# Kernel tuning notes

Hardware: AMD Instinct MI355X
Metric: run time of the kernel (lower is better)

## Reference

```python
import jax, jax.numpy as jnp
import numpy as np

B, T, E = 4, 2048, 1024
H = 16
D = E // H  # head_dim = 64


def setup_inputs() -> dict:
    key = jax.random.key(0)
    k1, k2, k3 = jax.random.split(key, 3)
    x = jax.random.normal(k1, (B, T, E), dtype=jnp.float32)
    # torch nn.Linear weights: y = x @ W.T ; init scaled like uniform fan_in
    W_qkv = jax.random.normal(k2, (3 * E, E), dtype=jnp.float32) * (E ** -0.5)
    W_out = jax.random.normal(k3, (E, E), dtype=jnp.float32) * (E ** -0.5)
    return {"x": x, "W_qkv": W_qkv, "W_out": W_out}


def reference(x, W_qkv, W_out):
    b, t, c = x.shape
    scale = D ** -0.5
    qkv = jnp.einsum('btc,fc->btf', x, W_qkv)          # [B,T,3E]
    q, k, v = jnp.split(qkv, 3, axis=-1)
    # [B,H,T,D]
    q = q.reshape(b, t, H, D).transpose(0, 2, 1, 3)
    k = k.reshape(b, t, H, D).transpose(0, 2, 1, 3)
    v = v.reshape(b, t, H, D).transpose(0, 2, 1, 3)
    attn = jnp.einsum('bhqd,bhkd->bhqk', q, k) * scale  # [B,H,T,T]
    causal = jnp.triu(jnp.ones((t, t), dtype=bool), k=1)
    attn = jnp.where(causal, -jnp.inf, attn)
    attn = jax.nn.softmax(attn, axis=-1)
    out = jnp.einsum('bhqk,bhkd->bhqd', attn, v)        # [B,H,T,D]
    out = out.transpose(0, 2, 1, 3).reshape(b, t, c)
    return jnp.einsum('btc,oc->bto', out, W_out)
```

## Files before the change

### kernel.cpp

```cpp
#include <hip/hip_runtime.h>

using u16 = unsigned short;
using u32 = unsigned int;
typedef __bf16 bf16;
typedef bf16 bf16x8 __attribute__((ext_vector_type(8)));
typedef u16 u16x8 __attribute__((ext_vector_type(8)));
typedef u16 u16x4 __attribute__((ext_vector_type(4)));
typedef u32 u32x2 __attribute__((ext_vector_type(2)));
typedef float f32x4 __attribute__((ext_vector_type(4)));

#define LDSS 72

__device__ __forceinline__ u16 f2bf(float f) {
  u32 u = __builtin_bit_cast(u32, f);
  u += 0x7FFFu + ((u >> 16) & 1u);
  return (u16)(u >> 16);
}

__device__ __forceinline__ u32 packtrunc(float lo, float hi) {
  return __builtin_amdgcn_perm(__builtin_bit_cast(u32, hi),
                               __builtin_bit_cast(u32, lo), 0x07060302u);
}

__device__ __forceinline__ float fexp2(float x) {
#if __has_builtin(__builtin_amdgcn_exp2f)
  return __builtin_amdgcn_exp2f(x);
#else
  return exp2f(x);
#endif
}

__device__ __forceinline__ bf16x8 ldfrag(const u16* p) {
  return __builtin_bit_cast(bf16x8, *(const u16x8*)p);
}

__device__ __forceinline__ u16x8 cvt8(const float* p) {
  float4 a = ((const float4*)p)[0];
  float4 b = ((const float4*)p)[1];
  u16x8 o;
  o[0] = f2bf(a.x); o[1] = f2bf(a.y); o[2] = f2bf(a.z); o[3] = f2bf(a.w);
  o[4] = f2bf(b.x); o[5] = f2bf(b.y); o[6] = f2bf(b.z); o[7] = f2bf(b.w);
  return o;
}

__device__ __forceinline__ void gll16(const u16* g, u16* l) {
  __builtin_amdgcn_global_load_lds(
      (const __attribute__((address_space(1))) u32*)g,
      (__attribute__((address_space(3))) u32*)l, 16, 0, 0);
}

__global__ __launch_bounds__(256) void cvt_bf16(
    const float* __restrict__ src, u16* __restrict__ dst, int n8) {
  int i = blockIdx.x * 256 + threadIdx.x;
  const int stride = gridDim.x * 256;
  for (; i < n8; i += stride)
    ((u16x8*)dst)[i] = cvt8(&src[(size_t)i * 8]);
}

template<int MODE, int NBX>
__global__ __launch_bounds__(512, 2) void gemm256(
    const u16* __restrict__ Ag, const u16* __restrict__ Bg,
    u16* __restrict__ Qw, u16* __restrict__ Kw, u16* __restrict__ Vtw,
    float* __restrict__ Og) {
  extern __shared__ u16 lds[];
  u16* Ab0 = lds;
  u16* Bb0 = lds + 16384;
  u16* Ab1 = lds + 32768;
  u16* Bb1 = lds + 49152;

  const int tid = threadIdx.x;
  const int lane = tid & 63;
  const int wid = tid >> 6;
  const int wm = wid >> 2, wn = wid & 3;
  const int quad = lane >> 4, l16 = lane & 15;
  const int row_off = lane >> 3;
  const int csrc = ((lane & 7) * 8) ^ (row_off << 3);
  const int swl = (l16 & 7) << 3;

  const int cpx = (NBX * 32) >> 3;
  const int bid = blockIdx.x;
  const int swz = (bid & 7) * cpx + (bid >> 3);
  const int by = swz / NBX, bx = swz % NBX;
  const int arow0 = by * 256, brow0 = bx * 256;

  f32x4 acc[8][4] = {};
  bf16x8 af[8];
  bf16x8 bfx[4];

  auto stg = [&](const u16* G, int grow0, u16* dst, int t, int h) {
#pragma unroll
    for (int q = 0; q < 2; ++q) {
      int r = h * 128 + q * 64 + wid * 8;
      gll16(&G[(size_t)(grow0 + r + row_off) * 1024 + t * 64 + csrc],
            &dst[r * 64]);
    }
  };

#define LOADA(BUF, MH) do { \
  _Pragma("unroll") for (int i2 = 0; i2 < 4; ++i2) \
  _Pragma("unroll") for (int kk = 0; kk < 2; ++kk) \
    af[i2*2+kk] = ldfrag(&BUF[(wm*128 + ((MH)*4+i2)*16 + l16)*64 + ((kk*32+quad*8) ^ swl)]); \
} while(0)

#define LOADB(BUF, NH) do { \
  _Pragma("unroll") for (int j2 = 0; j2 < 2; ++j2) \
  _Pragma("unroll") for (int kk = 0; kk < 2; ++kk) \
    bfx[j2*2+kk] = ldfrag(&BUF[(wn*64 + ((NH)*2+j2)*16 + l16)*64 + ((kk*32+quad*8) ^ swl)]); \
} while(0)

#define MFMAQ(MH, NH) do { \
  __builtin_amdgcn_s_setprio(1); \
  _Pragma("unroll") for (int i2 = 0; i2 < 4; ++i2) \
  _Pragma("unroll") for (int j2 = 0; j2 < 2; ++j2) \
  _Pragma("unroll") for (int kk = 0; kk < 2; ++kk) \
    acc[(MH)*4+i2][(NH)*2+j2] = __builtin_amdgcn_mfma_f32_16x16x32_bf16( \
        af[i2*2+kk], bfx[j2*2+kk], acc[(MH)*4+i2][(NH)*2+j2], 0, 0, 0); \
  __builtin_amdgcn_s_setprio(0); \
} while(0)

#define BARSYNC __builtin_amdgcn_s_barrier()
#define LGKM0 do { asm volatile("s_waitcnt lgkmcnt(0)" ::: "memory"); \
                   __builtin_amdgcn_sched_barrier(0); } while(0)

  stg(Ag, arow0, Ab0, 0, 0);
  stg(Bg, brow0, Bb0, 0, 1);
  stg(Ag, arow0, Ab0, 0, 1);
  stg(Bg, brow0, Bb0, 0, 0);
  stg(Ag, arow0, Ab1, 1, 0);
  stg(Bg, brow0, Bb1, 1, 1);
  asm volatile("s_waitcnt vmcnt(4)" ::: "memory");
  BARSYNC;

  for (int i = 0; i < 8; ++i) {
    const int t1 = 2 * i + 1, t2 = 2 * i + 2, t3 = 2 * i + 3;
    const bool more = (i < 7);
    LOADA(Ab0, 0); LOADB(Bb0, 0); stg(Ag, arow0, Ab1, t1, 1);
    BARSYNC; LGKM0; MFMAQ(0, 0); BARSYNC;
    LOADB(Bb0, 1); stg(Bg, brow0, Bb1, t1, 0);
    BARSYNC; LGKM0; MFMAQ(0, 1); BARSYNC;
    LOADA(Ab0, 1); if (more) stg(Ag, arow0, Ab0, t2, 0);
    BARSYNC; LGKM0; MFMAQ(1, 1); BARSYNC;
    LOADB(Bb0, 0);
    if (more) { stg(Bg, brow0, Bb0, t2, 1);
                asm volatile("s_waitcnt vmcnt(4)" ::: "memory"); }
    else      { asm volatile("s_waitcnt vmcnt(0)" ::: "memory"); }
    BARSYNC; LGKM0; MFMAQ(1, 0); BARSYNC;
    LOADA(Ab1, 0); LOADB(Bb1, 0); if (more) stg(Ag, arow0, Ab0, t2, 1);
    BARSYNC; LGKM0; MFMAQ(0, 0); BARSYNC;
    LOADB(Bb1, 1); if (more) stg(Bg, brow0, Bb0, t2, 0);
    BARSYNC; LGKM0; MFMAQ(0, 1); BARSYNC;
    LOADA(Ab1, 1); if (more) stg(Ag, arow0, Ab1, t3, 0);
    BARSYNC; LGKM0; MFMAQ(1, 1); BARSYNC;
    LOADB(Bb1, 0);
    if (more) { stg(Bg, brow0, Bb1, t3, 1);
                asm volatile("s_waitcnt vmcnt(4)" ::: "memory"); }
    BARSYNC; LGKM0; MFMAQ(1, 0); BARSYNC;
  }

  if constexpr (MODE == 0) {
    const int part = bx >> 2;
    const int h = (bx & 3) * 4 + wn;
    const int bb = by >> 3;
    const int tb0 = (by & 7) * 256 + wm * 128;
    if (part < 2) {
      u16* dst = part == 0 ? Qw : Kw;
      const float qs = part == 0 ? 0.18033688011112042f : 1.0f;
      const size_t rowb = (size_t)(bb * 16 + h) * 2048;
#pragma unroll
      for (int i2 = 0; i2 < 8; ++i2)
#pragma unroll
        for (int j2 = 0; j2 < 4; ++j2) {
          int t = tb0 + i2 * 16 + quad * 4;
          int d = j2 * 16 + l16;
#pragma unroll
          for (int r = 0; r < 4; ++r)
            dst[(rowb + t + r) * 64 + d] = f2bf(acc[i2][j2][r] * qs);
        }
    } else {
      __builtin_amdgcn_s_barrier();
      u16* tb = lds + wid * 8192;
      const int swt = l16 << 2;
#pragma unroll
      for (int i2 = 0; i2 < 8; ++i2)
#pragma unroll
        for (int j2 = 0; j2 < 4; ++j2) {
          u16x4 v4;
#pragma unroll
          for (int r = 0; r < 4; ++r) v4[r] = f2bf(acc[i2][j2][r]);
          int mb = i2 * 16 + quad * 4;
          *(u16x4*)&tb[(j2 * 16 + l16) * 128 + (mb ^ swt)] = v4;
        }
      asm volatile("s_waitcnt lgkmcnt(0)" ::: "memory");
      const int dl = lane;
      const int swr = (dl & 15) << 2;
      u16* vr = Vtw + ((size_t)(bb * 16 + h) * 64 + dl) * 2048 + tb0;
#pragma unroll
      for (int c = 0; c < 16; ++c) {
        u16x4 q0 = *(u16x4*)&tb[dl * 128 + ((c * 8) ^ swr)];
        u16x4 q1 = *(u16x4*)&tb[dl * 128 + ((c * 8 + 4) ^ swr)];
        u16x8 o;
        o[0] = q0[0]; o[1] = q0[1]; o[2] = q0[2]; o[3] = q0[3];
        o[4] = q1[0]; o[5] = q1[1]; o[6] = q1[2]; o[7] = q1[3];
        *(u16x8*)&vr[c * 8] = o;
      }
    }
  } else {
    const size_t mrow = (size_t)(by * 256 + wm * 128);
    const int ocol = bx * 256 + wn * 64;
#pragma unroll
    for (int i2 = 0; i2 < 8; ++i2)
#pragma unroll
      for (int j2 = 0; j2 < 4; ++j2)
#pragma unroll
        for (int r = 0; r < 4; ++r)
          Og[(mrow + i2 * 16 + quad * 4 + r) * 1024 + ocol + j2 * 16 + l16] =
              acc[i2][j2][r];
  }
#undef LOADA
#undef LOADB
#undef MFMAQ
#undef BARSYNC
#undef LGKM0
}

__global__ __launch_bounds__(256) void attn_kernel(
    const u16* __restrict__ Qw, const u16* __restrict__ Kw,
    const u16* __restrict__ Vtw, u16* __restrict__ Ao) {
  __shared__ u16 kbuf0[64 * 64], vbuf0[64 * 64];
  __shared__ u16 kbuf1[64 * 64], vbuf1[64 * 64];
  __shared__ u16 pws[4][32 * LDSS];
  const int tid = threadIdx.x;
  const int lane = tid & 63;
  const int wid = tid >> 6;
  const int quad = lane >> 4;
  const int l16 = lane & 15;
  const int g = 15 - (int)(blockIdx.x >> 6);
  const int bh = blockIdx.x & 63;
  const u16* Qb = Qw + (size_t)bh * 2048 * 64;
  const u16* Kb = Kw + (size_t)bh * 2048 * 64;
  const u16* Vb = Vtw + (size_t)bh * 64 * 2048;
  const int sw = 4 * g + wid;
  const int qrow0 = sw * 32;
  const int nktw = (sw >> 1) + 1;
  const int nkt = 2 * g + 2;
  u16* pw = pws[wid];

  const int lr = lane >> 3;
  const int lsw = ((lane & 7) * 8) ^ (lr << 3);
  const int sx = (l16 & 7) << 3;

  bf16x8 qf[2][2];
#pragma unroll
  for (int i = 0; i < 2; ++i)
#pragma unroll
    for (int kk = 0; kk < 2; ++kk)
      qf[i][kk] = ldfrag(&Qb[(size_t)(qrow0 + i * 16 + l16) * 64 + kk * 32 + quad * 8]);

  f32x4 oacc[4][2] = {};
  float mst[2] = {-INFINITY, -INFINITY};
  float lst[2] = {0.f, 0.f};

  auto stage = [&](int kt, u16* kb, u16* vb) {
    const u16* Kt = Kb + (size_t)kt * 4096;
    const u16* Vt = Vb + kt * 64;
#pragma unroll
    for (int c = 0; c < 2; ++c) {
      int base = wid * 1024 + c * 512;
      int rb = wid * 16 + c * 8;
      gll16(&Kt[(size_t)rb * 64 + lr * 64 + lsw], &kb[base]);
      gll16(&Vt[(size_t)rb * 2048 + lr * 2048 + lsw], &vb[base]);
    }
  };

  stage(0, kbuf0, vbuf0);

  auto body = [&](const u16* kc, const u16* vc, u16* kn, u16* vn, int kt) {
    asm volatile("s_waitcnt lgkmcnt(0)" ::: "memory");
    __builtin_amdgcn_s_barrier();
    const bool more = (kt + 1 < nkt);
    if (more) {
      stage(kt + 1, kn, vn);
      asm volatile("s_waitcnt vmcnt(4)" ::: "memory");
    } else {
      asm volatile("s_waitcnt vmcnt(0)" ::: "memory");
    }
    __builtin_amdgcn_s_barrier();
    if (kt >= nktw) return;

    f32x4 sv[2][4] = {};
    __builtin_amdgcn_s_setprio(1);
#pragma unroll
    for (int kk = 0; kk < 2; ++kk) {
      const int cq = (kk * 32 + quad * 8) ^ sx;
      bf16x8 kf[4];
#pragma unroll
      for (int j = 0; j < 4; ++j)
        kf[j] = ldfrag(&kc[(j * 16 + l16) * 64 + cq]);
#pragma unroll
      for (int i = 0; i < 2; ++i)
#pragma unroll
        for (int j = 0; j < 4; ++j)
          sv[i][j] = __builtin_amdgcn_mfma_f32_16x16x32_bf16(kf[j], qf[i][kk], sv[i][j], 0, 0, 0);
    }
    __builtin_amdgcn_s_setprio(0);

    if (kt * 64 + 63 > qrow0) {
#pragma unroll
      for (int i = 0; i < 2; ++i) {
        int q = qrow0 + i * 16 + l16;
#pragma unroll
        for (int j = 0; j < 4; ++j)
#pragma unroll
          for (int r = 0; r < 4; ++r)
            if (kt * 64 + j * 16 + quad * 4 + r > q) sv[i][j][r] = -INFINITY;
      }
    }

#pragma unroll
    for (int i = 0; i < 2; ++i) {
      float mx = -INFINITY;
#pragma unroll
      for (int j = 0; j < 4; ++j)
#pragma unroll
        for (int r = 0; r < 4; ++r) mx = fmaxf(mx, sv[i][j][r]);
      mx = fmaxf(mx, __shfl_xor(mx, 16));
      mx = fmaxf(mx, __shfl_xor(mx, 32));
      float mnew = fmaxf(mst[i], mx);
      if (!__all(mnew == mst[i])) {
        float alpha = fexp2(mst[i] - mnew);
        lst[i] *= alpha;
#pragma unroll
        for (int d = 0; d < 4; ++d) oacc[d][i] *= alpha;
        mst[i] = mnew;
      }
      float rs = 0.f;
#pragma unroll
      for (int j = 0; j < 4; ++j) {
        float p0 = fexp2(sv[i][j][0] - mst[i]);
        float p1 = fexp2(sv[i][j][1] - mst[i]);
        float p2 = fexp2(sv[i][j][2] - mst[i]);
        float p3 = fexp2(sv[i][j][3] - mst[i]);
        rs += (p0 + p1) + (p2 + p3);
        u32x2 pk;
        pk[0] = packtrunc(p0, p1);
        pk[1] = packtrunc(p2, p3);
        *(u32x2*)&pw[(i * 16 + l16) * LDSS + j * 16 + quad * 4] = pk;
      }
      rs += __shfl_xor(rs, 16);
      rs += __shfl_xor(rs, 32);
      lst[i] += rs;
    }

#pragma unroll
    for (int kk = 0; kk < 2; ++kk) {
      const int cq = (kk * 32 + quad * 8) ^ sx;
      bf16x8 pf[2];
#pragma unroll
      for (int i = 0; i < 2; ++i)
        pf[i] = ldfrag(&pw[(i * 16 + l16) * LDSS + kk * 32 + quad * 8]);
      __builtin_amdgcn_s_setprio(1);
#pragma unroll
      for (int d = 0; d < 4; ++d) {
        bf16x8 vfd = ldfrag(&vc[(d * 16 + l16) * 64 + cq]);
#pragma unroll
        for (int i = 0; i < 2; ++i)
          oacc[d][i] = __builtin_amdgcn_mfma_f32_16x16x32_bf16(vfd, pf[i], oacc[d][i], 0, 0, 0);
      }
      __builtin_amdgcn_s_setprio(0);
    }
  };

  for (int kt = 0; kt < nkt; kt += 2) {
    body(kbuf0, vbuf0, kbuf1, vbuf1, kt);
    body(kbuf1, vbuf1, kbuf0, vbuf0, kt + 1);
  }

  const int bb = bh >> 4, h = bh & 15;
#pragma unroll
  for (int i = 0; i < 2; ++i) {
    float inv = 1.f / lst[i];
#pragma unroll
    for (int d = 0; d < 4; ++d) {
      u16x4 ok;
#pragma unroll
      for (int r = 0; r < 4; ++r) ok[r] = f2bf(oacc[d][i][r] * inv);
      *(u16x4*)&pw[(i * 16 + l16) * LDSS + d * 16 + quad * 4] = ok;
    }
  }
  __builtin_amdgcn_s_waitcnt(0);
  const int row = lane >> 1, half = lane & 1;
  const int t = qrow0 + row;
#pragma unroll
  for (int c = 0; c < 4; ++c) {
    u16x8 v = *(u16x8*)&pw[row * LDSS + half * 32 + c * 8];
    *(u16x8*)&Ao[((size_t)(bb * 2048 + t)) * 1024 + h * 64 + half * 32 + c * 8] = v;
  }
}

extern "C" void kernel_launch(void* const* d_in, const int* in_sizes, int n_in,
                              void* d_out, int out_size, void* d_ws, size_t ws_size,
                              hipStream_t stream) {
  (void)in_sizes; (void)n_in; (void)out_size; (void)ws_size;
  const float* x    = (const float*)d_in[0];
  const float* Wqkv = (const float*)d_in[1];
  const float* Wout = (const float*)d_in[2];
  float* out = (float*)d_out;
  u16* ws = (u16*)d_ws;

  const size_t NX   = (size_t)4 * 2048 * 1024;
  const size_t NQKV = (size_t)3072 * 1024;
  const size_t NOUT = (size_t)1024 * 1024;
  const size_t SZ   = NX;

  u16* Xc    = ws;
  u16* Wqkvc = Xc + NX;
  u16* Woutc = Wqkvc + NQKV;
  u16* Qw    = Woutc + NOUT;
  u16* Kw    = Qw + SZ;
  u16* Vtw   = Kw + SZ;
  u16* Ao    = Vtw + SZ;

  static bool attr_done = false;
  if (!attr_done) {
    (void)hipFuncSetAttribute(reinterpret_cast<const void*>(&gemm256<0, 12>),
                              hipFuncAttributeMaxDynamicSharedMemorySize, 131072);
    (void)hipFuncSetAttribute(reinterpret_cast<const void*>(&gemm256<1, 4>),
                              hipFuncAttributeMaxDynamicSharedMemorySize, 131072);
    attr_done = true;
  }

  cvt_bf16<<<dim3(1024), 256, 0, stream>>>(x, Xc, (int)(NX / 8));
  cvt_bf16<<<dim3(384), 256, 0, stream>>>(Wqkv, Wqkvc, (int)(NQKV / 8));
  cvt_bf16<<<dim3(128), 256, 0, stream>>>(Wout, Woutc, (int)(NOUT / 8));

  gemm256<0, 12><<<dim3(384), 512, 131072, stream>>>(
      Xc, Wqkvc, Qw, Kw, Vtw, nullptr);
  attn_kernel<<<dim3(1024), 256, 0, stream>>>(Qw, Kw, Vtw, Ao);
  gemm256<1, 4><<<dim3(128), 512, 131072, stream>>>(
      Ao, Woutc, nullptr, nullptr, nullptr, out);
}
```

Before: 260.1 us.

## Shrink GEMM tiles to 128x256, simplify pipeline, widen attention blocks

The GEMM kernel changes from 256x256 tiles with a hand-interleaved quarter-step schedule to 128x256 tiles with a simple double-buffered loop, which doubles the grid for both projections and lowers register and LDS use. The attention kernel now runs 8 waves per block covering 256 query rows, with a reordered block-to-query-group mapping and half as many blocks. The aim is better CU fill and load balance, at the cost of less operand reuse per tile and coarser causal work per block.

```diff
diff --git a/kernel.cpp b/kernel.cpp
--- a/kernel.cpp
+++ b/kernel.cpp
@@ -58,157 +58,144 @@
 }
 
 template<int MODE, int NBX>
-__global__ __launch_bounds__(512, 2) void gemm256(
+__global__ __launch_bounds__(512) void gemm128(
     const u16* __restrict__ Ag, const u16* __restrict__ Bg,
     u16* __restrict__ Qw, u16* __restrict__ Kw, u16* __restrict__ Vtw,
     float* __restrict__ Og) {
   extern __shared__ u16 lds[];
   u16* Ab0 = lds;
-  u16* Bb0 = lds + 16384;
-  u16* Ab1 = lds + 32768;
-  u16* Bb1 = lds + 49152;
+  u16* Bb0 = lds + 8192;
+  u16* Ab1 = lds + 24576;
+  u16* Bb1 = lds + 32768;
 
   const int tid = threadIdx.x;
   const int lane = tid & 63;
   const int wid = tid >> 6;
   const int wm = wid >> 2, wn = wid & 3;
   const int quad = lane >> 4, l16 = lane & 15;
-  const int row_off = lane >> 3;
-  const int csrc = ((lane & 7) * 8) ^ (row_off << 3);
+  const int lr = lane >> 3;
+  const int csrc = ((lane & 7) * 8) ^ (lr << 3);
   const int swl = (l16 & 7) << 3;
 
-  const int cpx = (NBX * 32) >> 3;
+  const int nwg = NBX * 64;
+  const int cpx = nwg >> 3;
   const int bid = blockIdx.x;
   const int swz = (bid & 7) * cpx + (bid >> 3);
   const int by = swz / NBX, bx = swz % NBX;
-  const int arow0 = by * 256, brow0 = bx * 256;
-
-  f32x4 acc[8][4] = {};
-  bf16x8 af[8];
-  bf16x8 bfx[4];
-
-  auto stg = [&](const u16* G, int grow0, u16* dst, int t, int h) {
-#pragma unroll
-    for (int q = 0; q < 2; ++q) {
-      int r = h * 128 + q * 64 + wid * 8;
-      gll16(&G[(size_t)(grow0 + r + row_off) * 1024 + t * 64 + csrc],
-            &dst[r * 64]);
+  const int arow0 = by * 128, brow0 = bx * 256;
+
+  f32x4 acc[4][4] = {};
+
+  auto stg = [&](int t, u16* Abuf, u16* Bbuf) {
+#pragma unroll
+    for (int s2 = 0; s2 < 2; ++s2) {
+      int r = s2 * 64 + wid * 8;
+      gll16(&Ag[(size_t)(arow0 + r + lr) * 1024 + t * 64 + csrc], &Abuf[r * 64]);
+    }
+#pragma unroll
+    for (int s2 = 0; s2 < 4; ++s2) {
+      int r = s2 * 64 + wid * 8;
+      gll16(&Bg[(size_t)(brow0 + r + lr) * 1024 + t * 64 + csrc], &Bbuf[r * 64]);
     }
   };
 
-#define LOADA(BUF, MH) do { \
-  _Pragma("unroll") for (int i2 = 0; i2 < 4; ++i2) \
-  _Pragma("unroll") for (int kk = 0; kk < 2; ++kk) \
-    af[i2*2+kk] = ldfrag(&BUF[(wm*128 + ((MH)*4+i2)*16 + l16)*64 + ((kk*32+quad*8) ^ swl)]); \
-} while(0)
-
-#define LOADB(BUF, NH) do { \
-  _Pragma("unroll") for (int j2 = 0; j2 < 2; ++j2) \
-  _Pragma("unroll") for (int kk = 0; kk < 2; ++kk) \
-    bfx[j2*2+kk] = ldfrag(&BUF[(wn*64 + ((NH)*2+j2)*16 + l16)*64 + ((kk*32+quad*8) ^ swl)]); \
-} while(0)
-
-#define MFMAQ(MH, NH) do { \
-  __builtin_amdgcn_s_setprio(1); \
-  _Pragma("unroll") for (int i2 = 0; i2 < 4; ++i2) \
-  _Pragma("unroll") for (int j2 = 0; j2 < 2; ++j2) \
-  _Pragma("unroll") for (int kk = 0; kk < 2; ++kk) \
-    acc[(MH)*4+i2][(NH)*2+j2] = __builtin_amdgcn_mfma_f32_16x16x32_bf16( \
-        af[i2*2+kk], bfx[j2*2+kk], acc[(MH)*4+i2][(NH)*2+j2], 0, 0, 0); \
-  __builtin_amdgcn_s_setprio(0); \
-} while(0)
-
-#define BARSYNC __builtin_amdgcn_s_barrier()
-#define LGKM0 do { asm volatile("s_waitcnt lgkmcnt(0)" ::: "memory"); \
-                   __builtin_amdgcn_sched_barrier(0); } while(0)
-
-  stg(Ag, arow0, Ab0, 0, 0);
-  stg(Bg, brow0, Bb0, 0, 1);
-  stg(Ag, arow0, Ab0, 0, 1);
-  stg(Bg, brow0, Bb0, 0, 0);
-  stg(Ag, arow0, Ab1, 1, 0);
-  stg(Bg, brow0, Bb1, 1, 1);
-  asm volatile("s_waitcnt vmcnt(4)" ::: "memory");
-  BARSYNC;
-
-  for (int i = 0; i < 8; ++i) {
-    const int t1 = 2 * i + 1, t2 = 2 * i + 2, t3 = 2 * i + 3;
-    const bool more = (i < 7);
-    LOADA(Ab0, 0); LOADB(Bb0, 0); stg(Ag, arow0, Ab1, t1, 1);
-    BARSYNC; LGKM0; MFMAQ(0, 0); BARSYNC;
-    LOADB(Bb0, 1); stg(Bg, brow0, Bb1, t1, 0);
-    BARSYNC; LGKM0; MFMAQ(0, 1); BARSYNC;
-    LOADA(Ab0, 1); if (more) stg(Ag, arow0, Ab0, t2, 0);
-    BARSYNC; LGKM0; MFMAQ(1, 1); BARSYNC;
-    LOADB(Bb0, 0);
-    if (more) { stg(Bg, brow0, Bb0, t2, 1);
-                asm volatile("s_waitcnt vmcnt(4)" ::: "memory"); }
-    else      { asm volatile("s_waitcnt vmcnt(0)" ::: "memory"); }
-    BARSYNC; LGKM0; MFMAQ(1, 0); BARSYNC;
-    LOADA(Ab1, 0); LOADB(Bb1, 0); if (more) stg(Ag, arow0, Ab0, t2, 1);
-    BARSYNC; LGKM0; MFMAQ(0, 0); BARSYNC;
-    LOADB(Bb1, 1); if (more) stg(Bg, brow0, Bb0, t2, 0);
-    BARSYNC; LGKM0; MFMAQ(0, 1); BARSYNC;
-    LOADA(Ab1, 1); if (more) stg(Ag, arow0, Ab1, t3, 0);
-    BARSYNC; LGKM0; MFMAQ(1, 1); BARSYNC;
-    LOADB(Bb1, 0);
-    if (more) { stg(Bg, brow0, Bb1, t3, 1);
-                asm volatile("s_waitcnt vmcnt(4)" ::: "memory"); }
-    BARSYNC; LGKM0; MFMAQ(1, 0); BARSYNC;
+  stg(0, Ab0, Bb0);
+
+  auto body = [&](const u16* Ac, const u16* Bc, u16* An, u16* Bn, int t) {
+    asm volatile("s_waitcnt lgkmcnt(0)" ::: "memory");
+    __builtin_amdgcn_s_barrier();
+    if (t + 1 < 16) {
+      stg(t + 1, An, Bn);
+      asm volatile("s_waitcnt vmcnt(6)" ::: "memory");
+    } else {
+      asm volatile("s_waitcnt vmcnt(0)" ::: "memory");
+    }
+    __builtin_amdgcn_s_barrier();
+
+    bf16x8 bfx[8], af[4];
+#pragma unroll
+    for (int j2 = 0; j2 < 4; ++j2)
+#pragma unroll
+      for (int kk = 0; kk < 2; ++kk)
+        bfx[j2 * 2 + kk] = ldfrag(
+            &Bc[(wn * 64 + j2 * 16 + l16) * 64 + ((kk * 32 + quad * 8) ^ swl)]);
+#pragma unroll
+    for (int mh = 0; mh < 2; ++mh) {
+#pragma unroll
+      for (int i2 = 0; i2 < 2; ++i2)
+#pragma unroll
+        for (int kk = 0; kk < 2; ++kk)
+          af[i2 * 2 + kk] = ldfrag(
+              &Ac[(wm * 64 + (mh * 2 + i2) * 16 + l16) * 64 + ((kk * 32 + quad * 8) ^ swl)]);
+      __builtin_amdgcn_s_setprio(1);
+#pragma unroll
+      for (int i2 = 0; i2 < 2; ++i2)
+#pragma unroll
+        for (int j2 = 0; j2 < 4; ++j2)
+#pragma unroll
+          for (int kk = 0; kk < 2; ++kk)
+            acc[mh * 2 + i2][j2] = __builtin_amdgcn_mfma_f32_16x16x32_bf16(
+                af[i2 * 2 + kk], bfx[j2 * 2 + kk], acc[mh * 2 + i2][j2], 0, 0, 0);
+      __builtin_amdgcn_s_setprio(0);
+    }
+  };
+
+  for (int t = 0; t < 16; t += 2) {
+    body(Ab0, Bb0, Ab1, Bb1, t);
+    body(Ab1, Bb1, Ab0, Bb0, t + 1);
   }
 
   if constexpr (MODE == 0) {
     const int part = bx >> 2;
     const int h = (bx & 3) * 4 + wn;
-    const int bb = by >> 3;
-    const int tb0 = (by & 7) * 256 + wm * 128;
+    const int bb = by >> 4;
+    const int t0 = (by & 15) * 128 + wm * 64;
     if (part < 2) {
       u16* dst = part == 0 ? Qw : Kw;
       const float qs = part == 0 ? 0.18033688011112042f : 1.0f;
       const size_t rowb = (size_t)(bb * 16 + h) * 2048;
 #pragma unroll
-      for (int i2 = 0; i2 < 8; ++i2)
+      for (int i2 = 0; i2 < 4; ++i2)
 #pragma unroll
         for (int j2 = 0; j2 < 4; ++j2) {
-          int t = tb0 + i2 * 16 + quad * 4;
+          int tt = t0 + i2 * 16 + quad * 4;
           int d = j2 * 16 + l16;
 #pragma unroll
           for (int r = 0; r < 4; ++r)
-            dst[(rowb + t + r) * 64 + d] = f2bf(acc[i2][j2][r] * qs);
+            dst[(rowb + tt + r) * 64 + d] = f2bf(acc[i2][j2][r] * qs);
         }
     } else {
       __builtin_amdgcn_s_barrier();
-      u16* tb = lds + wid * 8192;
-      const int swt = l16 << 2;
-#pragma unroll
-      for (int i2 = 0; i2 < 8; ++i2)
+      u16* tb = lds + wid * 4096;
+#pragma unroll
+      for (int i2 = 0; i2 < 4; ++i2)
 #pragma unroll
         for (int j2 = 0; j2 < 4; ++j2) {
           u16x4 v4;
 #pragma unroll
           for (int r = 0; r < 4; ++r) v4[r] = f2bf(acc[i2][j2][r]);
           int mb = i2 * 16 + quad * 4;
-          *(u16x4*)&tb[(j2 * 16 + l16) * 128 + (mb ^ swt)] = v4;
+          *(u16x4*)&tb[(j2 * 16 + l16) * 64 + (mb ^ (l16 << 2))] = v4;
         }
       asm volatile("s_waitcnt lgkmcnt(0)" ::: "memory");
       const int dl = lane;
       const int swr = (dl & 15) << 2;
-      u16* vr = Vtw + ((size_t)(bb * 16 + h) * 64 + dl) * 2048 + tb0;
-#pragma unroll
-      for (int c = 0; c < 16; ++c) {
-        u16x4 q0 = *(u16x4*)&tb[dl * 128 + ((c * 8) ^ swr)];
-        u16x4 q1 = *(u16x4*)&tb[dl * 128 + ((c * 8 + 4) ^ swr)];
+      u16* vr = Vtw + ((size_t)(bb * 16 + h) * 64 + dl) * 2048 + t0;
+#pragma unroll
+      for (int c8 = 0; c8 < 8; ++c8) {
+        u16x4 q0 = *(u16x4*)&tb[dl * 64 + ((c8 * 8) ^ swr)];
+        u16x4 q1 = *(u16x4*)&tb[dl * 64 + ((c8 * 8 + 4) ^ swr)];
         u16x8 o;
         o[0] = q0[0]; o[1] = q0[1]; o[2] = q0[2]; o[3] = q0[3];
         o[4] = q1[0]; o[5] = q1[1]; o[6] = q1[2]; o[7] = q1[3];
-        *(u16x8*)&vr[c * 8] = o;
+        *(u16x8*)&vr[c8 * 8] = o;
       }
     }
   } else {
-    const size_t mrow = (size_t)(by * 256 + wm * 128);
-    const int ocol = bx * 256 + wn * 64;
-#pragma unroll
-    for (int i2 = 0; i2 < 8; ++i2)
+    const size_t mrow = (size_t)arow0 + wm * 64;
+    const int ocol = brow0 + wn * 64;
+#pragma unroll
+    for (int i2 = 0; i2 < 4; ++i2)
 #pragma unroll
       for (int j2 = 0; j2 < 4; ++j2)
 #pragma unroll
@@ -216,33 +203,29 @@
           Og[(mrow + i2 * 16 + quad * 4 + r) * 1024 + ocol + j2 * 16 + l16] =
               acc[i2][j2][r];
   }
-#undef LOADA
-#undef LOADB
-#undef MFMAQ
-#undef BARSYNC
-#undef LGKM0
-}
-
-__global__ __launch_bounds__(256) void attn_kernel(
+}
+
+__global__ __launch_bounds__(512) void attn_kernel(
     const u16* __restrict__ Qw, const u16* __restrict__ Kw,
     const u16* __restrict__ Vtw, u16* __restrict__ Ao) {
   __shared__ u16 kbuf0[64 * 64], vbuf0[64 * 64];
   __shared__ u16 kbuf1[64 * 64], vbuf1[64 * 64];
-  __shared__ u16 pws[4][32 * LDSS];
+  __shared__ u16 pws[8][32 * LDSS];
   const int tid = threadIdx.x;
   const int lane = tid & 63;
   const int wid = tid >> 6;
   const int quad = lane >> 4;
   const int l16 = lane & 15;
-  const int g = 15 - (int)(blockIdx.x >> 6);
+  const int idx = (int)(blockIdx.x >> 6);
+  const int g = idx < 4 ? 7 - idx : idx - 4;
   const int bh = blockIdx.x & 63;
   const u16* Qb = Qw + (size_t)bh * 2048 * 64;
   const u16* Kb = Kw + (size_t)bh * 2048 * 64;
   const u16* Vb = Vtw + (size_t)bh * 64 * 2048;
-  const int sw = 4 * g + wid;
-  const int qrow0 = sw * 32;
-  const int nktw = (sw >> 1) + 1;
-  const int nkt = 2 * g + 2;
+  const int sq = 8 * g + wid;
+  const int qrow0 = sq * 32;
+  const int nktw = (sq >> 1) + 1;
+  const int nkt = 4 * g + 4;
   u16* pw = pws[wid];
 
   const int lr = lane >> 3;
@@ -263,13 +246,9 @@
   auto stage = [&](int kt, u16* kb, u16* vb) {
     const u16* Kt = Kb + (size_t)kt * 4096;
     const u16* Vt = Vb + kt * 64;
-#pragma unroll
-    for (int c = 0; c < 2; ++c) {
-      int base = wid * 1024 + c * 512;
-      int rb = wid * 16 + c * 8;
-      gll16(&Kt[(size_t)rb * 64 + lr * 64 + lsw], &kb[base]);
-      gll16(&Vt[(size_t)rb * 2048 + lr * 2048 + lsw], &vb[base]);
-    }
+    const int rb = wid * 8;
+    gll16(&Kt[(size_t)(rb + lr) * 64 + lsw], &kb[wid * 512]);
+    gll16(&Vt[(size_t)(rb + lr) * 2048 + lsw], &vb[wid * 512]);
   };
 
   stage(0, kbuf0, vbuf0);
@@ -280,7 +259,7 @@
     const bool more = (kt + 1 < nkt);
     if (more) {
       stage(kt + 1, kn, vn);
-      asm volatile("s_waitcnt vmcnt(4)" ::: "memory");
+      asm volatile("s_waitcnt vmcnt(2)" ::: "memory");
     } else {
       asm volatile("s_waitcnt vmcnt(0)" ::: "memory");
     }
@@ -422,10 +401,10 @@
 
   static bool attr_done = false;
   if (!attr_done) {
-    (void)hipFuncSetAttribute(reinterpret_cast<const void*>(&gemm256<0, 12>),
-                              hipFuncAttributeMaxDynamicSharedMemorySize, 131072);
-    (void)hipFuncSetAttribute(reinterpret_cast<const void*>(&gemm256<1, 4>),
-                              hipFuncAttributeMaxDynamicSharedMemorySize, 131072);
+    (void)hipFuncSetAttribute(reinterpret_cast<const void*>(&gemm128<0, 12>),
+                              hipFuncAttributeMaxDynamicSharedMemorySize, 98304);
+    (void)hipFuncSetAttribute(reinterpret_cast<const void*>(&gemm128<1, 4>),
+                              hipFuncAttributeMaxDynamicSharedMemorySize, 98304);
     attr_done = true;
   }
 
@@ -433,9 +412,9 @@
   cvt_bf16<<<dim3(384), 256, 0, stream>>>(Wqkv, Wqkvc, (int)(NQKV / 8));
   cvt_bf16<<<dim3(128), 256, 0, stream>>>(Wout, Woutc, (int)(NOUT / 8));
 
-  gemm256<0, 12><<<dim3(384), 512, 131072, stream>>>(
+  gemm128<0, 12><<<dim3(768), 512, 98304, stream>>>(
       Xc, Wqkvc, Qw, Kw, Vtw, nullptr);
-  attn_kernel<<<dim3(1024), 256, 0, stream>>>(Qw, Kw, Vtw, Ao);
-  gemm256<1, 4><<<dim3(128), 512, 131072, stream>>>(
+  attn_kernel<<<dim3(512), 512, 0, stream>>>(Qw, Kw, Vtw, Ao);
+  gemm128<1, 4><<<dim3(256), 512, 98304, stream>>>(
       Ao, Woutc, nullptr, nullptr, nullptr, out);
 }
```

Measured after the change: 256.3 us. No clear change (-1.4%).
